# Optimization experiments

Hardware: AMD Instinct MI355X
Metric: run time of the kernel (lower is better)

## Reference

```python
import jax, jax.numpy as jnp
import numpy as np

B, C, H, W = 8, 256, 64, 64
D = C // 8  # query/key channels


def setup_inputs() -> dict:
    key = jax.random.key(0)
    ks = jax.random.split(key, 7)
    s = 0.05
    x = jax.random.normal(ks[0], (B, C, H, W), dtype=jnp.float32)
    Wq = jax.random.normal(ks[1], (D, C), dtype=jnp.float32) * s
    bq = jax.random.normal(ks[2], (D,), dtype=jnp.float32) * s
    Wk = jax.random.normal(ks[3], (D, C), dtype=jnp.float32) * s
    bk = jax.random.normal(ks[4], (D,), dtype=jnp.float32) * s
    Wv = jax.random.normal(ks[5], (C, C), dtype=jnp.float32) * s
    bv = jax.random.normal(ks[6], (C,), dtype=jnp.float32) * s
    return {"x": x, "Wq": Wq, "bq": bq, "Wk": Wk, "bk": bk, "Wv": Wv, "bv": bv}


def reference(x, Wq, bq, Wk, bk, Wv, bv):
    b, c, h, w = x.shape
    n = h * w
    xf = x.reshape(b, c, n)  # (B, C, HW)
    # 1x1 convs == per-pixel linear projections
    q = jnp.einsum('dc,bcn->bdn', Wq, xf) + bq[None, :, None]  # (B, D, HW)
    k = jnp.einsum('dc,bcn->bdn', Wk, xf) + bk[None, :, None]  # (B, D, HW)
    v = jnp.einsum('ec,bcn->ben', Wv, xf) + bv[None, :, None]  # (B, C, HW)
    # attention[b, n, m] = sum_d q[b,d,n] * k[b,d,m]  (no 1/sqrt(d) scaling)
    attn = jax.nn.softmax(jnp.einsum('bdn,bdm->bnm', q, k), axis=-1)
    # out[b,c,n] = sum_m v[b,c,m] * attn[b,n,m]  (v @ attn^T)
    out = jnp.einsum('bcm,bnm->bcn', v, attn)
    return out.reshape(b, c, h, w) + x
```

## Files before the change

### kernel.cpp

```cpp
#include <hip/hip_runtime.h>
#include <stdint.h>

#define BN 4096
#define NCH 256
#define DQ 32

typedef _Float16 half8  __attribute__((ext_vector_type(8)));
typedef _Float16 half4  __attribute__((ext_vector_type(4)));
typedef float   floatx4  __attribute__((ext_vector_type(4)));
typedef float   floatx16 __attribute__((ext_vector_type(16)));

typedef __attribute__((address_space(1))) const void g1_void;
typedef __attribute__((address_space(3))) void l3_void;

__global__ __launch_bounds__(256) void convert_w(
    const float* __restrict__ Wq, const float* __restrict__ Wk,
    const float* __restrict__ Wv, _Float16* __restrict__ W16)
{
    int e4 = (blockIdx.x * 256 + threadIdx.x) * 4;
    float4 v;
    if (e4 < 8192)        v = *(const float4*)&Wq[e4];
    else if (e4 < 16384)  v = *(const float4*)&Wk[e4 - 8192];
    else                  v = *(const float4*)&Wv[e4 - 16384];
    half4 h = { (_Float16)v.x, (_Float16)v.y, (_Float16)v.z, (_Float16)v.w };
    *(half4*)&W16[e4] = h;
}

__global__ __launch_bounds__(512) void proj_kernel(
    const float* __restrict__ x, const _Float16* __restrict__ W16,
    const float* __restrict__ bq, const float* __restrict__ bk,
    const float* __restrict__ bv,
    _Float16* __restrict__ qT, _Float16* __restrict__ kT,
    _Float16* __restrict__ vb)
{
    const int t  = threadIdx.x;
    const int n0 = blockIdx.x * 128;
    const int b  = blockIdx.y;

    __shared__ __align__(16) _Float16 xTl[128 * 256];

#pragma unroll
    for (int p = 0; p < 2; ++p) {
        const int kb = p * 128 + (t >> 5) * 8;
        const int n4 = (t & 31) * 4;
        float4 xr[8];
#pragma unroll
        for (int i = 0; i < 8; ++i)
            xr[i] = *(const float4*)&x[((size_t)b * NCH + kb + i) * BN + n0 + n4];
        const float* xf = (const float*)xr;
#pragma unroll
        for (int j = 0; j < 4; ++j) {
            const int n = n4 + j;
            half8 hv;
#pragma unroll
            for (int i = 0; i < 8; ++i) hv[i] = (_Float16)xf[i * 4 + j];
            const int phys = (kb >> 3) ^ ((n >> 2) & 31);
            *(half8*)&xTl[n * 256 + phys * 8] = hv;
        }
    }
    __syncthreads();

    const int lane  = t & 63;
    const int w     = t >> 6;
    const int col32 = lane & 31;
    const int h     = lane >> 5;
    const int nc    = w & 3;
    const int job   = w >> 2;

    const _Float16* Wq16 = W16;
    const _Float16* Wk16 = W16 + 8192;
    const _Float16* Wv16 = W16 + 16384;

#define XFRAG(ks) (*(const half8*)&xTl[(nc * 32 + col32) * 256 + \
        (((ks) * 2 + h) ^ (((nc * 32 + col32) >> 2) & 31)) * 8])

    if (job == 0) {
        const float bqv = bq[col32];
        const float bkv = bk[col32];
        floatx16 aq, ak2;
#pragma unroll
        for (int r = 0; r < 16; ++r) { aq[r] = 0.0f; ak2[r] = 0.0f; }
#pragma unroll
        for (int ks = 0; ks < 16; ++ks) {
            half8 xa = XFRAG(ks);
            half8 wqf = *(const half8*)&Wq16[col32 * 256 + ks * 16 + h * 8];
            half8 wkf = *(const half8*)&Wk16[col32 * 256 + ks * 16 + h * 8];
            aq  = __builtin_amdgcn_mfma_f32_32x32x16_f16(xa, wqf, aq, 0, 0, 0);
            ak2 = __builtin_amdgcn_mfma_f32_32x32x16_f16(xa, wkf, ak2, 0, 0, 0);
        }
#pragma unroll
        for (int r = 0; r < 16; ++r) {
            const int n = n0 + nc * 32 + (r & 3) + 8 * (r >> 2) + 4 * h;
            qT[((size_t)b * BN + n) * DQ + col32] = (_Float16)(aq[r] + bqv);
            kT[((size_t)b * BN + n) * DQ + col32] = (_Float16)(ak2[r] + bkv);
        }
    }

    const int rg_lo = (job == 0) ? 0 : 3;
    const int rg_hi = (job == 0) ? 3 : 8;
    for (int rg = rg_lo; rg < rg_hi; ++rg) {
        floatx16 av;
#pragma unroll
        for (int r = 0; r < 16; ++r) av[r] = 0.0f;
#pragma unroll
        for (int ks = 0; ks < 16; ++ks) {
            half8 xb  = XFRAG(ks);
            half8 wvf = *(const half8*)&Wv16[(rg * 32 + col32) * 256 + ks * 16 + h * 8];
            av = __builtin_amdgcn_mfma_f32_32x32x16_f16(wvf, xb, av, 0, 0, 0);
        }
#pragma unroll
        for (int r = 0; r < 16; ++r) {
            const int c = rg * 32 + (r & 3) + 8 * (r >> 2) + 4 * h;
            vb[((size_t)b * NCH + c) * BN + n0 + nc * 32 + col32] =
                (_Float16)(av[r] + bv[c]);
        }
    }
#undef XFRAG
}

__global__ __launch_bounds__(256, 3) void flash_kernel(
    const _Float16* __restrict__ qT, const _Float16* __restrict__ kT,
    const _Float16* __restrict__ vb,
    _Float16* __restrict__ Op, float* __restrict__ Ml)
{
    const int t    = threadIdx.x;
    const int lane = t & 63;
    const int w    = t >> 6;
    const int n0   = blockIdx.x * 64;
    const int kh   = blockIdx.y;
    const int b    = blockIdx.z;
    const int kbase = kh * 2048;

    __shared__ __align__(16) _Float16 vs[NCH * 64];
    __shared__ __align__(16) _Float16 Ps[64 * 64];
    __shared__ float alph_s[64];
    __shared__ float l_s[64];

    const int col   = lane & 15;
    const int q4    = lane >> 4;
    const int col32 = lane & 31;
    const int h     = lane >> 5;

    const _Float16* kp = kT + (size_t)b * BN * DQ;
    const _Float16* vp = vb + (size_t)b * NCH * BN;

    half8 bqf = *(const half8*)&qT[((size_t)b * BN + n0 + w * 16 + col) * DQ + q4 * 8];

    floatx16 acc[2][2];
#pragma unroll
    for (int ct = 0; ct < 2; ++ct)
#pragma unroll
        for (int nt = 0; nt < 2; ++nt)
#pragma unroll
            for (int r = 0; r < 16; ++r) acc[ct][nt][r] = 0.0f;

    float m_i = -1e30f, l_i = 0.0f;

    const int sc_loc = lane >> 3;
    const int s_log  = (lane & 7) ^ (sc_loc & 7);
    half8 ak[4];
#pragma unroll
    for (int mt = 0; mt < 4; ++mt)
        ak[mt] = *(const half8*)&kp[(size_t)(kbase + mt * 16 + col) * DQ + q4 * 8];
#pragma unroll
    for (int j = 0; j < 8; ++j) {
        const int c = w * 64 + j * 8 + sc_loc;
        __builtin_amdgcn_global_load_lds(
            (g1_void*)&vp[(size_t)c * BN + kbase + s_log * 8],
            (l3_void*)&vs[(w * 64 + j * 8) * 64], 16, 0, 0);
    }

    for (int it = 0; it < 32; ++it) {
        const int mc = kbase + it * 64;

        floatx4 sf[4];
#pragma unroll
        for (int mt = 0; mt < 4; ++mt) {
            floatx4 z = { 0.0f, 0.0f, 0.0f, 0.0f };
            sf[mt] = __builtin_amdgcn_mfma_f32_16x16x32_f16(ak[mt], bqf, z, 0, 0, 0);
        }

        float cmax = -1e30f;
#pragma unroll
        for (int mt = 0; mt < 4; ++mt)
#pragma unroll
            for (int r = 0; r < 4; ++r) cmax = fmaxf(cmax, sf[mt][r]);
        cmax = fmaxf(cmax, __shfl_xor(cmax, 16));
        cmax = fmaxf(cmax, __shfl_xor(cmax, 32));
        float mn = fmaxf(m_i, cmax);
        float al = __expf(m_i - mn);
        float csum = 0.0f;
        half4 pk[4];
#pragma unroll
        for (int mt = 0; mt < 4; ++mt) {
            float p0 = __expf(sf[mt][0] - mn);
            float p1 = __expf(sf[mt][1] - mn);
            float p2 = __expf(sf[mt][2] - mn);
            float p3 = __expf(sf[mt][3] - mn);
            csum += p0 + p1 + p2 + p3;
            pk[mt] = (half4){ (_Float16)p0, (_Float16)p1, (_Float16)p2, (_Float16)p3 };
        }
        csum += __shfl_xor(csum, 16);
        csum += __shfl_xor(csum, 32);
        l_i = l_i * al + csum;
        m_i = mn;

        {
            const int n = w * 16 + col;
#pragma unroll
            for (int mt = 0; mt < 4; ++mt) {
                const int p_log = 2 * mt + (q4 >> 1);
                const int p_phys = p_log ^ (n & 7);
                *(half4*)((char*)&Ps[n * 64] + p_phys * 16 + (q4 & 1) * 8) = pk[mt];
            }
            if (q4 == 0) alph_s[n] = al;
        }

        __syncthreads();

        float a0 = alph_s[col32];
        float a1 = alph_s[32 + col32];
#pragma unroll
        for (int ct = 0; ct < 2; ++ct)
#pragma unroll
            for (int r = 0; r < 16; ++r) {
                acc[ct][0][r] *= a0;
                acc[ct][1][r] *= a1;
            }

#pragma unroll
        for (int ks = 0; ks < 4; ++ks) {
            const int p_log = 2 * ks + h;
            half8 bp0 = *(const half8*)((char*)&Ps[col32 * 64] + (p_log ^ (col32 & 7)) * 16);
            half8 bp1 = *(const half8*)((char*)&Ps[(32 + col32) * 64] + (p_log ^ (col32 & 7)) * 16);
#pragma unroll
            for (int ct = 0; ct < 2; ++ct) {
                const int c = w * 64 + ct * 32 + col32;
                half8 av = *(const half8*)((char*)&vs[c * 64] + ((p_log ^ (c & 7)) * 16));
                acc[ct][0] = __builtin_amdgcn_mfma_f32_32x32x16_f16(av, bp0, acc[ct][0], 0, 0, 0);
                acc[ct][1] = __builtin_amdgcn_mfma_f32_32x32x16_f16(av, bp1, acc[ct][1], 0, 0, 0);
            }
        }

        __syncthreads();

        if (it < 31) {
            const int mcn = mc + 64;
#pragma unroll
            for (int mt = 0; mt < 4; ++mt)
                ak[mt] = *(const half8*)&kp[(size_t)(mcn + mt * 16 + col) * DQ + q4 * 8];
#pragma unroll
            for (int j = 0; j < 8; ++j) {
                const int c = w * 64 + j * 8 + sc_loc;
                __builtin_amdgcn_global_load_lds(
                    (g1_void*)&vp[(size_t)c * BN + mcn + s_log * 8],
                    (l3_void*)&vs[(w * 64 + j * 8) * 64], 16, 0, 0);
            }
        }
    }

    if (q4 == 0) {
        const int n = n0 + w * 16 + col;
        Ml[(size_t)(kh * 8 + b) * BN + n] = m_i;
        Ml[(size_t)(16 + kh * 8 + b) * BN + n] = l_i;
    }
    _Float16* Opp = Op + (size_t)(kh * 8 + b) * NCH * BN;
#pragma unroll
    for (int ct = 0; ct < 2; ++ct)
#pragma unroll
        for (int nt = 0; nt < 2; ++nt)
#pragma unroll
            for (int r = 0; r < 16; ++r) {
                int row = (r & 3) + 8 * (r >> 2) + 4 * h;
                int c = w * 64 + ct * 32 + row;
                Opp[(size_t)c * BN + n0 + nt * 32 + col32] = (_Float16)acc[ct][nt][r];
            }
}

__global__ __launch_bounds__(256) void combine_kernel(
    const _Float16* __restrict__ Op, const float* __restrict__ Ml,
    const float* __restrict__ x, float* __restrict__ out)
{
    const int n = blockIdx.x * 256 + threadIdx.x;
    const int c0 = blockIdx.y * 16;
    const int b = blockIdx.z;

    const float m0 = Ml[(size_t)b * BN + n];
    const float m1 = Ml[(size_t)(8 + b) * BN + n];
    const float l0 = Ml[(size_t)(16 + b) * BN + n];
    const float l1 = Ml[(size_t)(24 + b) * BN + n];
    const float M = fmaxf(m0, m1);
    const float a0 = __expf(m0 - M);
    const float a1 = __expf(m1 - M);
    const float inv = 1.0f / (l0 * a0 + l1 * a1);
    const float f0 = a0 * inv;
    const float f1 = a1 * inv;

    const _Float16* Op0 = Op + (size_t)b * NCH * BN;
    const _Float16* Op1 = Op + (size_t)(8 + b) * NCH * BN;
#pragma unroll 4
    for (int ci = 0; ci < 16; ++ci) {
        const int c = c0 + ci;
        const size_t off = ((size_t)b * NCH + c) * BN + n;
        const size_t po = (size_t)c * BN + n;
        out[off] = (float)Op0[po] * f0 + (float)Op1[po] * f1 + x[off];
    }
}

extern "C" void kernel_launch(void* const* d_in, const int* in_sizes, int n_in,
                              void* d_out, int out_size, void* d_ws, size_t ws_size,
                              hipStream_t stream)
{
    const float* x  = (const float*)d_in[0];
    const float* Wq = (const float*)d_in[1];
    const float* bq = (const float*)d_in[2];
    const float* Wk = (const float*)d_in[3];
    const float* bk = (const float*)d_in[4];
    const float* Wv = (const float*)d_in[5];
    const float* bv = (const float*)d_in[6];
    float* out = (float*)d_out;

    _Float16* ws = (_Float16*)d_ws;
    _Float16* W16 = ws;
    _Float16* qT  = W16 + 81920;
    _Float16* kT  = qT + (size_t)8 * BN * DQ;
    _Float16* vb  = kT + (size_t)8 * BN * DQ;
    _Float16* Op  = vb + (size_t)8 * NCH * BN;
    float*    Ml  = (float*)(Op + (size_t)2 * 8 * NCH * BN);

    convert_w<<<dim3(80), 256, 0, stream>>>(Wq, Wk, Wv, W16);
    proj_kernel<<<dim3(32, 8), 512, 0, stream>>>(x, W16, bq, bk, bv, qT, kT, vb);
    flash_kernel<<<dim3(BN / 64, 2, 8), 256, 0, stream>>>(qT, kT, vb, Op, Ml);
    combine_kernel<<<dim3(16, 16, 8), 256, 0, stream>>>(Op, Ml, x, out);
}
```

Before: 254.8 us.

## Double-buffer V and P tiles with smaller key tile, fold log2e into K

The flash kernel now uses 32-key tiles with double-buffered V, P and alpha shared buffers. This removes the second barrier per iteration and lets the next tile's V and K loads be issued before the PV MFMAs. Log2(e) is folded into Wk and bk so softmax can use exp2 directly, and the accumulator rescale is skipped when every alpha in the wave is 1. The cost is twice as many iterations, with one barrier and one softmax reduction each, and a K projection stored in fp16 with the extra scale applied.

```diff
diff --git a/kernel.cpp b/kernel.cpp
--- a/kernel.cpp
+++ b/kernel.cpp
@@ -13,6 +13,9 @@
 typedef __attribute__((address_space(1))) const void g1_void;
 typedef __attribute__((address_space(3))) void l3_void;
 
+#define LOG2E 1.44269504088896f
+#define EXP2F(x) __builtin_amdgcn_exp2f(x)
+
 __global__ __launch_bounds__(256) void convert_w(
     const float* __restrict__ Wq, const float* __restrict__ Wk,
     const float* __restrict__ Wv, _Float16* __restrict__ W16)
@@ -20,7 +23,10 @@
     int e4 = (blockIdx.x * 256 + threadIdx.x) * 4;
     float4 v;
     if (e4 < 8192)        v = *(const float4*)&Wq[e4];
-    else if (e4 < 16384)  v = *(const float4*)&Wk[e4 - 8192];
+    else if (e4 < 16384) {
+        v = *(const float4*)&Wk[e4 - 8192];
+        v.x *= LOG2E; v.y *= LOG2E; v.z *= LOG2E; v.w *= LOG2E;
+    }
     else                  v = *(const float4*)&Wv[e4 - 16384];
     half4 h = { (_Float16)v.x, (_Float16)v.y, (_Float16)v.z, (_Float16)v.w };
     *(half4*)&W16[e4] = h;
@@ -76,7 +82,7 @@
 
     if (job == 0) {
         const float bqv = bq[col32];
-        const float bkv = bk[col32];
+        const float bkv = bk[col32] * LOG2E;
         floatx16 aq, ak2;
 #pragma unroll
         for (int r = 0; r < 16; ++r) { aq[r] = 0.0f; ak2[r] = 0.0f; }
@@ -131,10 +137,9 @@
     const int b    = blockIdx.z;
     const int kbase = kh * 2048;
 
-    __shared__ __align__(16) _Float16 vs[NCH * 64];
-    __shared__ __align__(16) _Float16 Ps[64 * 64];
-    __shared__ float alph_s[64];
-    __shared__ float l_s[64];
+    __shared__ __align__(16) _Float16 vs[2][NCH * 32];
+    __shared__ __align__(16) _Float16 Ps[2][64 * 32];
+    __shared__ float alph_s[2][64];
 
     const int col   = lane & 15;
     const int q4    = lane >> 4;
@@ -156,47 +161,45 @@
 
     float m_i = -1e30f, l_i = 0.0f;
 
-    const int sc_loc = lane >> 3;
-    const int s_log  = (lane & 7) ^ (sc_loc & 7);
-    half8 ak[4];
-#pragma unroll
-    for (int mt = 0; mt < 4; ++mt)
-        ak[mt] = *(const half8*)&kp[(size_t)(kbase + mt * 16 + col) * DQ + q4 * 8];
-#pragma unroll
-    for (int j = 0; j < 8; ++j) {
-        const int c = w * 64 + j * 8 + sc_loc;
+    const int vrow_l = lane >> 2;
+#pragma unroll
+    for (int j = 0; j < 4; ++j) {
+        const int c = w * 64 + j * 16 + vrow_l;
+        const int s_log = (lane & 3) ^ ((c >> 1) & 3);
         __builtin_amdgcn_global_load_lds(
             (g1_void*)&vp[(size_t)c * BN + kbase + s_log * 8],
-            (l3_void*)&vs[(w * 64 + j * 8) * 64], 16, 0, 0);
-    }
-
-    for (int it = 0; it < 32; ++it) {
-        const int mc = kbase + it * 64;
-
-        floatx4 sf[4];
-#pragma unroll
-        for (int mt = 0; mt < 4; ++mt) {
+            (l3_void*)&vs[0][(w * 64 + j * 16) * 32], 16, 0, 0);
+    }
+    half8 ak[2];
+#pragma unroll
+    for (int mt = 0; mt < 2; ++mt)
+        ak[mt] = *(const half8*)&kp[(size_t)(kbase + mt * 16 + col) * DQ + q4 * 8];
+
+    for (int it = 0; it < 64; ++it) {
+        const int cur = it & 1;
+        const int mc  = kbase + it * 32;
+
+        floatx4 sf[2];
+#pragma unroll
+        for (int mt = 0; mt < 2; ++mt) {
             floatx4 z = { 0.0f, 0.0f, 0.0f, 0.0f };
             sf[mt] = __builtin_amdgcn_mfma_f32_16x16x32_f16(ak[mt], bqf, z, 0, 0, 0);
         }
 
-        float cmax = -1e30f;
-#pragma unroll
-        for (int mt = 0; mt < 4; ++mt)
-#pragma unroll
-            for (int r = 0; r < 4; ++r) cmax = fmaxf(cmax, sf[mt][r]);
+        float cmax = fmaxf(fmaxf(fmaxf(sf[0][0], sf[0][1]), fmaxf(sf[0][2], sf[0][3])),
+                           fmaxf(fmaxf(sf[1][0], sf[1][1]), fmaxf(sf[1][2], sf[1][3])));
         cmax = fmaxf(cmax, __shfl_xor(cmax, 16));
         cmax = fmaxf(cmax, __shfl_xor(cmax, 32));
         float mn = fmaxf(m_i, cmax);
-        float al = __expf(m_i - mn);
+        float al = EXP2F(m_i - mn);
         float csum = 0.0f;
-        half4 pk[4];
-#pragma unroll
-        for (int mt = 0; mt < 4; ++mt) {
-            float p0 = __expf(sf[mt][0] - mn);
-            float p1 = __expf(sf[mt][1] - mn);
-            float p2 = __expf(sf[mt][2] - mn);
-            float p3 = __expf(sf[mt][3] - mn);
+        half4 pk[2];
+#pragma unroll
+        for (int mt = 0; mt < 2; ++mt) {
+            float p0 = EXP2F(sf[mt][0] - mn);
+            float p1 = EXP2F(sf[mt][1] - mn);
+            float p2 = EXP2F(sf[mt][2] - mn);
+            float p3 = EXP2F(sf[mt][3] - mn);
             csum += p0 + p1 + p2 + p3;
             pk[mt] = (half4){ (_Float16)p0, (_Float16)p1, (_Float16)p2, (_Float16)p3 };
         }
@@ -207,54 +210,57 @@
 
         {
             const int n = w * 16 + col;
-#pragma unroll
-            for (int mt = 0; mt < 4; ++mt) {
-                const int p_log = 2 * mt + (q4 >> 1);
-                const int p_phys = p_log ^ (n & 7);
-                *(half4*)((char*)&Ps[n * 64] + p_phys * 16 + (q4 & 1) * 8) = pk[mt];
+            const int swz = (n >> 1) & 3;
+#pragma unroll
+            for (int mt = 0; mt < 2; ++mt) {
+                const int seg16 = mt * 2 + (q4 >> 1);
+                *(half4*)((char*)&Ps[cur][n * 32] + ((seg16 ^ swz) * 16 + (q4 & 1) * 8)) = pk[mt];
             }
-            if (q4 == 0) alph_s[n] = al;
+            if (q4 == 0) alph_s[cur][n] = al;
         }
 
         __syncthreads();
 
-        float a0 = alph_s[col32];
-        float a1 = alph_s[32 + col32];
-#pragma unroll
-        for (int ct = 0; ct < 2; ++ct)
-#pragma unroll
-            for (int r = 0; r < 16; ++r) {
-                acc[ct][0][r] *= a0;
-                acc[ct][1][r] *= a1;
+        if (it < 63) {
+            const int mcn = mc + 32;
+#pragma unroll
+            for (int j = 0; j < 4; ++j) {
+                const int c = w * 64 + j * 16 + vrow_l;
+                const int s_log = (lane & 3) ^ ((c >> 1) & 3);
+                __builtin_amdgcn_global_load_lds(
+                    (g1_void*)&vp[(size_t)c * BN + mcn + s_log * 8],
+                    (l3_void*)&vs[1 - cur][(w * 64 + j * 16) * 32], 16, 0, 0);
             }
-
-#pragma unroll
-        for (int ks = 0; ks < 4; ++ks) {
-            const int p_log = 2 * ks + h;
-            half8 bp0 = *(const half8*)((char*)&Ps[col32 * 64] + (p_log ^ (col32 & 7)) * 16);
-            half8 bp1 = *(const half8*)((char*)&Ps[(32 + col32) * 64] + (p_log ^ (col32 & 7)) * 16);
+#pragma unroll
+            for (int mt = 0; mt < 2; ++mt)
+                ak[mt] = *(const half8*)&kp[(size_t)(mcn + mt * 16 + col) * DQ + q4 * 8];
+        }
+
+        float a0 = alph_s[cur][col32];
+        float a1 = alph_s[cur][32 + col32];
+        if (!__all((a0 == 1.0f) && (a1 == 1.0f))) {
+#pragma unroll
+            for (int ct = 0; ct < 2; ++ct)
+#pragma unroll
+                for (int r = 0; r < 16; ++r) {
+                    acc[ct][0][r] *= a0;
+                    acc[ct][1][r] *= a1;
+                }
+        }
+
+        const int swz0 = (col32 >> 1) & 3;
+        const int swz1 = ((32 + col32) >> 1) & 3;
+#pragma unroll
+        for (int ks = 0; ks < 2; ++ks) {
+            const int seg = ks * 2 + h;
+            half8 bp0 = *(const half8*)((char*)&Ps[cur][col32 * 32] + (seg ^ swz0) * 16);
+            half8 bp1 = *(const half8*)((char*)&Ps[cur][(32 + col32) * 32] + (seg ^ swz1) * 16);
 #pragma unroll
             for (int ct = 0; ct < 2; ++ct) {
                 const int c = w * 64 + ct * 32 + col32;
-                half8 av = *(const half8*)((char*)&vs[c * 64] + ((p_log ^ (c & 7)) * 16));
+                half8 av = *(const half8*)((char*)&vs[cur][c * 32] + ((seg ^ ((c >> 1) & 3)) * 16));
                 acc[ct][0] = __builtin_amdgcn_mfma_f32_32x32x16_f16(av, bp0, acc[ct][0], 0, 0, 0);
                 acc[ct][1] = __builtin_amdgcn_mfma_f32_32x32x16_f16(av, bp1, acc[ct][1], 0, 0, 0);
-            }
-        }
-
-        __syncthreads();
-
-        if (it < 31) {
-            const int mcn = mc + 64;
-#pragma unroll
-            for (int mt = 0; mt < 4; ++mt)
-                ak[mt] = *(const half8*)&kp[(size_t)(mcn + mt * 16 + col) * DQ + q4 * 8];
-#pragma unroll
-            for (int j = 0; j < 8; ++j) {
-                const int c = w * 64 + j * 8 + sc_loc;
-                __builtin_amdgcn_global_load_lds(
-                    (g1_void*)&vp[(size_t)c * BN + mcn + s_log * 8],
-                    (l3_void*)&vs[(w * 64 + j * 8) * 64], 16, 0, 0);
             }
         }
     }
@@ -290,8 +296,8 @@
     const float l0 = Ml[(size_t)(16 + b) * BN + n];
     const float l1 = Ml[(size_t)(24 + b) * BN + n];
     const float M = fmaxf(m0, m1);
-    const float a0 = __expf(m0 - M);
-    const float a1 = __expf(m1 - M);
+    const float a0 = EXP2F(m0 - M);
+    const float a1 = EXP2F(m1 - M);
     const float inv = 1.0f / (l0 * a0 + l1 * a1);
     const float f0 = a0 * inv;
     const float f1 = a1 * inv;
```

Result: slower. 274.3 us (+7.7%).

## Add optional three-way key split, exp2 softmax and lazy rescaling in flash attention

Applied to the files above, without the earlier changes.

Folds log2(e) into the key weights and bias so the softmax can use the native exp2 instruction. It skips the accumulator rescale when every alpha in the wave equals one. When the workspace is large enough, keys are split three ways instead of two (1408 keys per split) to get more blocks and better occupancy. Each split now normalises its own output and stores a single log-sum-exp, so combine reads one value per split. This adds a third partial-output buffer to write and read, and the key weights are rounded to fp16 after the log2(e) scaling.

```diff
diff --git a/kernel.cpp b/kernel.cpp
--- a/kernel.cpp
+++ b/kernel.cpp
@@ -13,6 +13,10 @@
 typedef __attribute__((address_space(1))) const void g1_void;
 typedef __attribute__((address_space(3))) void l3_void;
 
+#define LOG2E 1.44269504088896f
+#define EXP2F(x) __builtin_amdgcn_exp2f(x)
+#define LOG2F(x) __builtin_amdgcn_logf(x)
+
 __global__ __launch_bounds__(256) void convert_w(
     const float* __restrict__ Wq, const float* __restrict__ Wk,
     const float* __restrict__ Wv, _Float16* __restrict__ W16)
@@ -20,7 +24,10 @@
     int e4 = (blockIdx.x * 256 + threadIdx.x) * 4;
     float4 v;
     if (e4 < 8192)        v = *(const float4*)&Wq[e4];
-    else if (e4 < 16384)  v = *(const float4*)&Wk[e4 - 8192];
+    else if (e4 < 16384) {
+        v = *(const float4*)&Wk[e4 - 8192];
+        v.x *= LOG2E; v.y *= LOG2E; v.z *= LOG2E; v.w *= LOG2E;
+    }
     else                  v = *(const float4*)&Wv[e4 - 16384];
     half4 h = { (_Float16)v.x, (_Float16)v.y, (_Float16)v.z, (_Float16)v.w };
     *(half4*)&W16[e4] = h;
@@ -76,7 +83,7 @@
 
     if (job == 0) {
         const float bqv = bq[col32];
-        const float bkv = bk[col32];
+        const float bkv = bk[col32] * LOG2E;
         floatx16 aq, ak2;
 #pragma unroll
         for (int r = 0; r < 16; ++r) { aq[r] = 0.0f; ak2[r] = 0.0f; }
@@ -121,7 +128,7 @@
 __global__ __launch_bounds__(256, 3) void flash_kernel(
     const _Float16* __restrict__ qT, const _Float16* __restrict__ kT,
     const _Float16* __restrict__ vb,
-    _Float16* __restrict__ Op, float* __restrict__ Ml)
+    _Float16* __restrict__ Op, float* __restrict__ Ml, int KPS)
 {
     const int t    = threadIdx.x;
     const int lane = t & 63;
@@ -129,7 +136,8 @@
     const int n0   = blockIdx.x * 64;
     const int kh   = blockIdx.y;
     const int b    = blockIdx.z;
-    const int kbase = kh * 2048;
+    const int kbase = kh * KPS;
+    const int iters = (min(KPS, BN - kbase)) >> 6;
 
     __shared__ __align__(16) _Float16 vs[NCH * 64];
     __shared__ __align__(16) _Float16 Ps[64 * 64];
@@ -170,7 +178,7 @@
             (l3_void*)&vs[(w * 64 + j * 8) * 64], 16, 0, 0);
     }
 
-    for (int it = 0; it < 32; ++it) {
+    for (int it = 0; it < iters; ++it) {
         const int mc = kbase + it * 64;
 
         floatx4 sf[4];
@@ -188,15 +196,15 @@
         cmax = fmaxf(cmax, __shfl_xor(cmax, 16));
         cmax = fmaxf(cmax, __shfl_xor(cmax, 32));
         float mn = fmaxf(m_i, cmax);
-        float al = __expf(m_i - mn);
+        float al = EXP2F(m_i - mn);
         float csum = 0.0f;
         half4 pk[4];
 #pragma unroll
         for (int mt = 0; mt < 4; ++mt) {
-            float p0 = __expf(sf[mt][0] - mn);
-            float p1 = __expf(sf[mt][1] - mn);
-            float p2 = __expf(sf[mt][2] - mn);
-            float p3 = __expf(sf[mt][3] - mn);
+            float p0 = EXP2F(sf[mt][0] - mn);
+            float p1 = EXP2F(sf[mt][1] - mn);
+            float p2 = EXP2F(sf[mt][2] - mn);
+            float p3 = EXP2F(sf[mt][3] - mn);
             csum += p0 + p1 + p2 + p3;
             pk[mt] = (half4){ (_Float16)p0, (_Float16)p1, (_Float16)p2, (_Float16)p3 };
         }
@@ -220,13 +228,15 @@
 
         float a0 = alph_s[col32];
         float a1 = alph_s[32 + col32];
-#pragma unroll
-        for (int ct = 0; ct < 2; ++ct)
-#pragma unroll
-            for (int r = 0; r < 16; ++r) {
-                acc[ct][0][r] *= a0;
-                acc[ct][1][r] *= a1;
-            }
+        if (!__all((a0 == 1.0f) && (a1 == 1.0f))) {
+#pragma unroll
+            for (int ct = 0; ct < 2; ++ct)
+#pragma unroll
+                for (int r = 0; r < 16; ++r) {
+                    acc[ct][0][r] *= a0;
+                    acc[ct][1][r] *= a1;
+                }
+        }
 
 #pragma unroll
         for (int ks = 0; ks < 4; ++ks) {
@@ -244,7 +254,7 @@
 
         __syncthreads();
 
-        if (it < 31) {
+        if (it + 1 < iters) {
             const int mcn = mc + 64;
 #pragma unroll
             for (int mt = 0; mt < 4; ++mt)
@@ -260,50 +270,57 @@
     }
 
     if (q4 == 0) {
-        const int n = n0 + w * 16 + col;
-        Ml[(size_t)(kh * 8 + b) * BN + n] = m_i;
-        Ml[(size_t)(16 + kh * 8 + b) * BN + n] = l_i;
-    }
+        const int n = w * 16 + col;
+        l_s[n] = l_i;
+        Ml[(size_t)(kh * 8 + b) * BN + n0 + n] = m_i + LOG2F(l_i);
+    }
+    __syncthreads();
+    const float li0 = 1.0f / l_s[col32];
+    const float li1 = 1.0f / l_s[32 + col32];
+
     _Float16* Opp = Op + (size_t)(kh * 8 + b) * NCH * BN;
 #pragma unroll
     for (int ct = 0; ct < 2; ++ct)
 #pragma unroll
-        for (int nt = 0; nt < 2; ++nt)
+        for (int nt = 0; nt < 2; ++nt) {
+            const float li = nt ? li1 : li0;
 #pragma unroll
             for (int r = 0; r < 16; ++r) {
                 int row = (r & 3) + 8 * (r >> 2) + 4 * h;
                 int c = w * 64 + ct * 32 + row;
-                Opp[(size_t)c * BN + n0 + nt * 32 + col32] = (_Float16)acc[ct][nt][r];
+                Opp[(size_t)c * BN + n0 + nt * 32 + col32] = (_Float16)(acc[ct][nt][r] * li);
             }
+        }
 }
 
 __global__ __launch_bounds__(256) void combine_kernel(
     const _Float16* __restrict__ Op, const float* __restrict__ Ml,
-    const float* __restrict__ x, float* __restrict__ out)
+    const float* __restrict__ x, float* __restrict__ out, int nsplit)
 {
     const int n = blockIdx.x * 256 + threadIdx.x;
     const int c0 = blockIdx.y * 16;
     const int b = blockIdx.z;
 
-    const float m0 = Ml[(size_t)b * BN + n];
-    const float m1 = Ml[(size_t)(8 + b) * BN + n];
-    const float l0 = Ml[(size_t)(16 + b) * BN + n];
-    const float l1 = Ml[(size_t)(24 + b) * BN + n];
-    const float M = fmaxf(m0, m1);
-    const float a0 = __expf(m0 - M);
-    const float a1 = __expf(m1 - M);
-    const float inv = 1.0f / (l0 * a0 + l1 * a1);
-    const float f0 = a0 * inv;
-    const float f1 = a1 * inv;
-
-    const _Float16* Op0 = Op + (size_t)b * NCH * BN;
-    const _Float16* Op1 = Op + (size_t)(8 + b) * NCH * BN;
+    float z[3], f[3];
+    float Z = -1e30f;
+    for (int s = 0; s < nsplit; ++s) {
+        z[s] = Ml[(size_t)(s * 8 + b) * BN + n];
+        Z = fmaxf(Z, z[s]);
+    }
+    float lsum = 0.0f;
+    for (int s = 0; s < nsplit; ++s) { f[s] = EXP2F(z[s] - Z); lsum += f[s]; }
+    const float inv = 1.0f / lsum;
+    for (int s = 0; s < nsplit; ++s) f[s] *= inv;
+
 #pragma unroll 4
     for (int ci = 0; ci < 16; ++ci) {
         const int c = c0 + ci;
         const size_t off = ((size_t)b * NCH + c) * BN + n;
         const size_t po = (size_t)c * BN + n;
-        out[off] = (float)Op0[po] * f0 + (float)Op1[po] * f1 + x[off];
+        float ov = 0.0f;
+        for (int s = 0; s < nsplit; ++s)
+            ov += (float)Op[(size_t)(s * 8 + b) * NCH * BN + po] * f[s];
+        out[off] = ov + x[off];
     }
 }
 
@@ -326,10 +343,18 @@
     _Float16* kT  = qT + (size_t)8 * BN * DQ;
     _Float16* vb  = kT + (size_t)8 * BN * DQ;
     _Float16* Op  = vb + (size_t)8 * NCH * BN;
-    float*    Ml  = (float*)(Op + (size_t)2 * 8 * NCH * BN);
+
+    const size_t baseElems = 81920 + (size_t)2 * 8 * BN * DQ + (size_t)8 * NCH * BN;
+    const size_t opElems3  = (size_t)3 * 8 * NCH * BN;
+    const size_t mlBytes   = (size_t)24 * BN * sizeof(float);
+    const size_t need3     = (baseElems + opElems3) * 2 + mlBytes + 256;
+    const int nsplit = (ws_size >= need3) ? 3 : 2;
+    const int KPS    = (nsplit == 3) ? 1408 : 2048;
+
+    float* Ml = (float*)(Op + (size_t)nsplit * 8 * NCH * BN);
 
     convert_w<<<dim3(80), 256, 0, stream>>>(Wq, Wk, Wv, W16);
     proj_kernel<<<dim3(32, 8), 512, 0, stream>>>(x, W16, bq, bk, bv, qT, kT, vb);
-    flash_kernel<<<dim3(BN / 64, 2, 8), 256, 0, stream>>>(qT, kT, vb, Op, Ml);
-    combine_kernel<<<dim3(16, 16, 8), 256, 0, stream>>>(Op, Ml, x, out);
-}
+    flash_kernel<<<dim3(64, nsplit, 8), 256, 0, stream>>>(qT, kT, vb, Op, Ml, KPS);
+    combine_kernel<<<dim3(16, 16, 8), 256, 0, stream>>>(Op, Ml, x, out, nsplit);
+}
```

Result: no change. 250.9 us (-1.5%).
